# Kernel optimization log

Measured on AMD Instinct MI355X. Metric: run time of the kernel, lower is better.

Reference implementation:

```python
import jax, jax.numpy as jnp
import numpy as np

D = 1024
H = 16
HD = D // H
EPS = 1e-5


def setup_inputs() -> dict:
    key = jax.random.key(0)
    ks = jax.random.split(key, 8)
    s_in = 1.0 / np.sqrt(D)
    s_ff = 1.0 / np.sqrt(4 * D)
    return {
        "x": jax.random.normal(ks[0], (2, 2048, D), dtype=jnp.float32),
        "w_qkv": jax.random.uniform(ks[1], (D, 3 * D), minval=-s_in, maxval=s_in, dtype=jnp.float32),
        "b_qkv": jnp.zeros((3 * D,), jnp.float32),
        "w_out": jax.random.uniform(ks[2], (D, D), minval=-s_in, maxval=s_in, dtype=jnp.float32),
        "b_out": jnp.zeros((D,), jnp.float32),
        "w_ff1": jax.random.uniform(ks[3], (D, 4 * D), minval=-s_in, maxval=s_in, dtype=jnp.float32),
        "b_ff1": jnp.zeros((4 * D,), jnp.float32),
        "w_ff2": jax.random.uniform(ks[4], (4 * D, D), minval=-s_ff, maxval=s_ff, dtype=jnp.float32),
        "b_ff2": jnp.zeros((D,), jnp.float32),
        "gamma1": jnp.ones((D,), jnp.float32),
        "beta1": jnp.zeros((D,), jnp.float32),
        "gamma2": jnp.ones((D,), jnp.float32),
        "beta2": jnp.zeros((D,), jnp.float32),
    }


def _layer_norm(x, gamma, beta):
    mean = jnp.mean(x, axis=-1, keepdims=True)
    var = jnp.var(x, axis=-1, keepdims=True, ddof=1)  # torch.var is unbiased
    return (x - mean) / jnp.sqrt(var + EPS) * gamma + beta


def reference(x, w_qkv, b_qkv, w_out, b_out, w_ff1, b_ff1, w_ff2, b_ff2,
              gamma1, beta1, gamma2, beta2):
    B, C, _ = x.shape
    qkv = x @ w_qkv + b_qkv                     # [B,C,3D]
    q, k, v = jnp.split(qkv, 3, axis=-1)
    # [B,C,D] -> [B,H,C,hd]
    q = q.reshape(B, C, H, HD).transpose(0, 2, 1, 3)
    k = k.reshape(B, C, H, HD).transpose(0, 2, 1, 3)
    v = v.reshape(B, C, H, HD).transpose(0, 2, 1, 3)
    attn = jnp.einsum('bhid,bhjd->bhij', q, k) / np.sqrt(HD).astype(np.float32)
    attn = jax.nn.softmax(attn, axis=-1)
    h_attn = jnp.einsum('bhij,bhjd->bhid', attn, v)
    h_attn = h_attn.transpose(0, 2, 1, 3).reshape(B, C, D)
    h_attn = h_attn @ w_out + b_out
    h_attn = _layer_norm(h_attn + x, gamma1, beta1)
    h_ff = jax.nn.gelu(h_attn @ w_ff1 + b_ff1, approximate=False) @ w_ff2 + b_ff2
    return _layer_norm(h_ff + h_attn, gamma2, beta2)
```

## Files before the change

kernel.cpp:

```cpp
#include <hip/hip_runtime.h>
#include <hip/hip_bf16.h>
#include <math.h>

#define DDIM 1024
#define HHD  64
#define NH   16
#define BB   2
#define CTX  2048
#define MROWS (BB*CTX)
#define D3   (3*DDIM)
#define DF   (4*DDIM)

using bf16x8 = __attribute__((ext_vector_type(8))) short;
using f32x4  = __attribute__((ext_vector_type(4))) float;

__device__ __forceinline__ unsigned short f2bf(float f) {
  union { float f; unsigned u; } c; c.f = f;
  unsigned u = c.u;
  return (unsigned short)((u + 0x7FFFu + ((u >> 16) & 1u)) >> 16);
}

__device__ __forceinline__ unsigned pk2(float a, float b) {
  __hip_bfloat162 h = __float22bfloat162_rn(float2{a, b});
  return *reinterpret_cast<unsigned*>(&h);
}

__device__ __forceinline__ void gload16(const void* g, void* l) {
  __builtin_amdgcn_global_load_lds(
      (const __attribute__((address_space(1))) unsigned int*)g,
      (__attribute__((address_space(3))) unsigned int*)l, 16, 0, 0);
}

template<int N>
__device__ __forceinline__ void vmwait() {
  if constexpr (N == 0)      asm volatile("s_waitcnt vmcnt(0)" ::: "memory");
  else if constexpr (N == 3) asm volatile("s_waitcnt vmcnt(3)" ::: "memory");
  else if constexpr (N == 4) asm volatile("s_waitcnt vmcnt(4)" ::: "memory");
  else static_assert(N != N, "add vmcnt literal");
}

__global__ void k_cvt_bf16(const float* __restrict__ in, unsigned short* __restrict__ out, int n4) {
  int i = blockIdx.x * blockDim.x + threadIdx.x;
  if (i >= n4) return;
  float4 v = reinterpret_cast<const float4*>(in)[i];
  uint2 o;
  o.x = pk2(v.x, v.y); o.y = pk2(v.z, v.w);
  reinterpret_cast<uint2*>(out)[i] = o;
}

__global__ void k_transpose_w(const float* __restrict__ in, unsigned short* __restrict__ out,
                              int R, int Cn) {
  __shared__ float tile[32][33];
  int c0 = blockIdx.x * 32, r0 = blockIdx.y * 32;
  int t = threadIdx.x, tr = t >> 5, tc = t & 31;
#pragma unroll
  for (int i = 0; i < 4; ++i)
    tile[tr + i*8][tc] = in[(size_t)(r0 + tr + i*8) * Cn + (c0 + tc)];
  __syncthreads();
#pragma unroll
  for (int i = 0; i < 4; ++i)
    out[(size_t)(c0 + tr + i*8) * R + (r0 + tc)] = f2bf(tile[tc][tr + i*8]);
}

__global__ void k_transpose_v(const unsigned short* __restrict__ in, unsigned short* __restrict__ out) {
  __shared__ unsigned short tile[32][33];
  int head = blockIdx.z;
  int d0 = blockIdx.x * 32, c0 = blockIdx.y * 32;
  int t = threadIdx.x, tr = t >> 5, tc = t & 31;
  const unsigned short* ip = in + (size_t)head * CTX * HHD;
  unsigned short* op = out + (size_t)head * CTX * HHD;
#pragma unroll
  for (int i = 0; i < 4; ++i)
    tile[tr + i*8][tc] = ip[(c0 + tr + i*8) * HHD + (d0 + tc)];
  __syncthreads();
#pragma unroll
  for (int i = 0; i < 4; ++i)
    op[(d0 + tr + i*8) * CTX + (c0 + tc)] = tile[tc][tr + i*8];
}

template<int EPI, int BM, int BN, int WSM, int WSN, int OCC>
__launch_bounds__(WSM*WSN*64, OCC)
__global__ void k_gemm(const unsigned short* __restrict__ A,
                       const unsigned short* __restrict__ Bt,
                       const float* __restrict__ bias,
                       const float* __restrict__ res,
                       float* __restrict__ outf,
                       unsigned short* __restrict__ outb,
                       unsigned short* __restrict__ outQ,
                       unsigned short* __restrict__ outK,
                       unsigned short* __restrict__ outV,
                       int Ndim, int Kdim) {
  constexpr int THREADS = WSM * WSN * 64;
  constexpr int WM = BM / (WSM * 16);
  constexpr int WN = BN / (WSN * 16);
  constexpr int LA = (BM * 4) / THREADS;
  constexpr int LB = (BN * 4) / THREADS;
  constexpr int L  = LA + LB;
  constexpr int NBUF = 3;

  __shared__ __align__(16) unsigned short As[NBUF][BM * 32];
  __shared__ __align__(16) unsigned short Bs[NBUF][BN * 32];

  const int nwg = gridDim.x * gridDim.y;
  const int lin = blockIdx.y * gridDim.x + blockIdx.x;
  const int swz = (lin & 7) * (nwg >> 3) + (lin >> 3);
  const int m0 = (swz / gridDim.x) * BM, n0 = (swz % gridDim.x) * BN;

  const int t = threadIdx.x;
  const int w = t >> 6, lane = t & 63, lr = lane & 15, lg = lane >> 4;
  const int wr = (w / WSN) * (WM * 16);
  const int wc = (w % WSN) * (WN * 16);

  f32x4 acc[WM][WN];
#pragma unroll
  for (int i = 0; i < WM; ++i)
#pragma unroll
    for (int j = 0; j < WN; ++j) acc[i][j] = f32x4{0.f, 0.f, 0.f, 0.f};

  const int srow = t >> 2;
  const int sgr  = (t & 3) ^ ((t >> 3) & 3);
  const unsigned short* Asrc[LA];
  const unsigned short* Bsrc[LB];
#pragma unroll
  for (int i = 0; i < LA; ++i)
    Asrc[i] = A + (size_t)(m0 + i * (THREADS / 4) + srow) * Kdim + sgr * 8;
#pragma unroll
  for (int i = 0; i < LB; ++i)
    Bsrc[i] = Bt + (size_t)(n0 + i * (THREADS / 4) + srow) * Kdim + sgr * 8;

  int offA[WM], offB[WN];
#pragma unroll
  for (int mi = 0; mi < WM; ++mi) {
    int r = wr + mi * 16 + lr;
    offA[mi] = r * 32 + ((lg ^ ((r >> 1) & 3)) * 8);
  }
#pragma unroll
  for (int ni = 0; ni < WN; ++ni) {
    int r = wc + ni * 16 + lr;
    offB[ni] = r * 32 + ((lg ^ ((r >> 1) & 3)) * 8);
  }

#define STAGE(buf, ko)                                                   \
  do {                                                                   \
    _Pragma("unroll")                                                    \
    for (int i = 0; i < LA; ++i)                                         \
      gload16(Asrc[i] + (ko), &As[buf][(i * THREADS + t) * 8]);          \
    _Pragma("unroll")                                                    \
    for (int i = 0; i < LB; ++i)                                         \
      gload16(Bsrc[i] + (ko), &Bs[buf][(i * THREADS + t) * 8]);          \
  } while (0)

  STAGE(0, 0);
  STAGE(1, 32);

  const int nk = Kdim >> 5;
  int rd = 0, tgt = 2;
  for (int kk = 0; kk < nk; ++kk) {
    if (kk + 1 < nk) vmwait<L>(); else vmwait<0>();
    __builtin_amdgcn_s_barrier();
    asm volatile("" ::: "memory");
    if (kk + 2 < nk) STAGE(tgt, (kk + 2) * 32);

    bf16x8 af[WM], bfr[WN];
#pragma unroll
    for (int mi = 0; mi < WM; ++mi) af[mi]  = *(const bf16x8*)&As[rd][offA[mi]];
#pragma unroll
    for (int ni = 0; ni < WN; ++ni) bfr[ni] = *(const bf16x8*)&Bs[rd][offB[ni]];
    if constexpr (WM >= 8) __builtin_amdgcn_s_setprio(1);
#pragma unroll
    for (int mi = 0; mi < WM; ++mi)
#pragma unroll
      for (int ni = 0; ni < WN; ++ni)
        acc[mi][ni] = __builtin_amdgcn_mfma_f32_16x16x32_bf16(af[mi], bfr[ni], acc[mi][ni], 0, 0, 0);
    if constexpr (WM >= 8) __builtin_amdgcn_s_setprio(0);
    rd  = (rd == 2)  ? 0 : rd + 1;
    tgt = (tgt == 2) ? 0 : tgt + 1;
  }
#undef STAGE

#pragma unroll
  for (int mi = 0; mi < WM; ++mi) {
#pragma unroll
    for (int r = 0; r < 4; ++r) {
      int row = m0 + wr + mi * 16 + lg * 4 + r;
#pragma unroll
      for (int ni = 0; ni < WN; ++ni) {
        int col = n0 + wc + ni * 16 + lr;
        float v = acc[mi][ni][r] + bias[col];
        if constexpr (EPI == 0) {
          int b = row >> 11, c = row & 2047;
          int sec = col >> 10, nn = col & 1023;
          int h = nn >> 6, d = nn & 63;
          size_t o = ((size_t)(b * NH + h) * CTX + c) * HHD + d;
          if (sec == 0) outQ[o] = f2bf(v * 0.18033688f);
          else if (sec == 1) outK[o] = f2bf(v);
          else outV[o] = f2bf(v);
        } else if constexpr (EPI == 1) {
          size_t o = (size_t)row * Ndim + col;
          outf[o] = v + res[o];
        } else {
          float g = 0.5f * v * (1.0f + erff(v * 0.70710678118654752f));
          outb[(size_t)row * Ndim + col] = f2bf(g);
        }
      }
    }
  }
}

__launch_bounds__(256, 4)
__global__ void k_attn(const unsigned short* __restrict__ Qb,
                       const unsigned short* __restrict__ Kb,
                       const unsigned short* __restrict__ Vt,
                       unsigned short* __restrict__ A2) {
  __shared__ __align__(16) unsigned short Ks[2][64 * 64];
  __shared__ __align__(16) unsigned short Vs[2][64 * 64];
  __shared__ __align__(16) unsigned short pls[4][16 * 64];
  const int lin = blockIdx.x;
  const int blk = (lin & 7) * 128 + (lin >> 3);
  const int bh = blk >> 5;
  const int qt = blk & 31;
  const int b = bh >> 4, h = bh & 15;
  const int t = threadIdx.x, w = t >> 6, lane = t & 63, lr = lane & 15, lg = lane >> 4;
  const int qbase = qt * 64 + w * 16;
  const unsigned short* Qh = Qb + (size_t)bh * CTX * HHD;
  const unsigned short* Kh = Kb + (size_t)bh * CTX * HHD;
  const unsigned short* Vh = Vt + (size_t)bh * CTX * HHD;
  unsigned short* pw = pls[w];

  const int srow = t >> 3, sgr = (t & 7) ^ ((t >> 3) & 7);
  const unsigned short* Kg0 = Kh + srow * HHD + sgr * 8;
  const unsigned short* Kg1 = Kg0 + 32 * HHD;
  const unsigned short* Vg0 = Vh + (size_t)srow * CTX + sgr * 8;
  const unsigned short* Vg1 = Vg0 + (size_t)32 * CTX;

#define STAGEKV(buf, j0)                              \
  do {                                                \
    gload16(Kg0 + (j0) * HHD, &Ks[buf][t * 8]);       \
    gload16(Kg1 + (j0) * HHD, &Ks[buf][(256 + t) * 8]); \
    gload16(Vg0 + (j0), &Vs[buf][t * 8]);             \
    gload16(Vg1 + (j0), &Vs[buf][(256 + t) * 8]);     \
  } while (0)

  STAGEKV(0, 0);

  bf16x8 aq[2];
#pragma unroll
  for (int kc = 0; kc < 2; ++kc)
    aq[kc] = *(const bf16x8*)(Qh + (qbase + lr) * HHD + kc * 32 + lg * 8);

  __syncthreads();

  float mrun = -1e30f, lsum = 0.f;
  f32x4 oacc[4];
#pragma unroll
  for (int nt = 0; nt < 4; ++nt) oacc[nt] = f32x4{0.f, 0.f, 0.f, 0.f};

  int cur = 0;
  for (int j0 = 0; j0 < CTX; j0 += 64) {
    if (j0 + 64 < CTX) STAGEKV(cur ^ 1, j0 + 64);

    f32x4 s[4];
#pragma unroll
    for (int nt = 0; nt < 4; ++nt) {
      s[nt] = f32x4{0.f, 0.f, 0.f, 0.f};
#pragma unroll
      for (int kc = 0; kc < 2; ++kc) {
        bf16x8 kf = *(const bf16x8*)&Ks[cur][(nt*16 + lr) * 64 + (((kc*4 + lg) ^ (lr & 7)) * 8)];
        s[nt] = __builtin_amdgcn_mfma_f32_16x16x32_bf16(kf, aq[kc], s[nt], 0, 0, 0);
      }
    }

    f32x4 m4;
#pragma unroll
    for (int r = 0; r < 4; ++r)
      m4[r] = fmaxf(fmaxf(s[0][r], s[1][r]), fmaxf(s[2][r], s[3][r]));
    float pm = fmaxf(fmaxf(m4[0], m4[1]), fmaxf(m4[2], m4[3]));
    if (__any(pm - mrun > 8.0f)) {
      float m = pm;
      m = fmaxf(m, __shfl_xor(m, 16));
      m = fmaxf(m, __shfl_xor(m, 32));
      float mn = fmaxf(mrun, m);
      float alpha = __builtin_amdgcn_exp2f(mrun - mn);
      mrun = mn;
      lsum *= alpha;
#pragma unroll
      for (int nt = 0; nt < 4; ++nt) oacc[nt] *= alpha;
    }
#pragma unroll
    for (int nt = 0; nt < 4; ++nt)
#pragma unroll
      for (int r = 0; r < 4; ++r)
        s[nt][r] = __builtin_amdgcn_exp2f(s[nt][r] - mrun);
    f32x4 s4 = (s[0] + s[1]) + (s[2] + s[3]);
    lsum += (s4[0] + s4[1]) + (s4[2] + s4[3]);

#pragma unroll
    for (int nt = 0; nt < 4; ++nt) {
      uint2 pk;
      pk.x = pk2(s[nt][0], s[nt][1]);
      pk.y = pk2(s[nt][2], s[nt][3]);
      int G = nt * 2 + (lg >> 1);
      *(uint2*)&pw[lr * 64 + ((G ^ (lr & 7)) * 8) + (lg & 1) * 4] = pk;
    }
    bf16x8 pf[2];
#pragma unroll
    for (int kc = 0; kc < 2; ++kc)
      pf[kc] = *(const bf16x8*)&pw[lr * 64 + (((kc*4 + lg) ^ (lr & 7)) * 8)];
#pragma unroll
    for (int nt = 0; nt < 4; ++nt) {
#pragma unroll
      for (int kc = 0; kc < 2; ++kc) {
        bf16x8 vf = *(const bf16x8*)&Vs[cur][(nt*16 + lr) * 64 + (((kc*4 + lg) ^ (lr & 7)) * 8)];
        oacc[nt] = __builtin_amdgcn_mfma_f32_16x16x32_bf16(vf, pf[kc], oacc[nt], 0, 0, 0);
      }
    }
    __syncthreads();
    cur ^= 1;
  }
#undef STAGEKV

  lsum += __shfl_xor(lsum, 16);
  lsum += __shfl_xor(lsum, 32);
  float rinv = 1.0f / lsum;
  size_t rowoff = ((size_t)(b * CTX + qbase + lr)) * DDIM + h * HHD;
#pragma unroll
  for (int nt = 0; nt < 4; ++nt) {
    uint2 ov;
    ov.x = pk2(oacc[nt][0] * rinv, oacc[nt][1] * rinv);
    ov.y = pk2(oacc[nt][2] * rinv, oacc[nt][3] * rinv);
    *(uint2*)&A2[rowoff + nt * 16 + lg * 4] = ov;
  }
}

template<bool WB>
__global__ void k_ln(const float* __restrict__ in, const float* __restrict__ gamma,
                     const float* __restrict__ beta, float* __restrict__ outf,
                     unsigned short* __restrict__ outb) {
  const int row = blockIdx.x, t = threadIdx.x;
  float4 v = reinterpret_cast<const float4*>(in + (size_t)row * DDIM)[t];
  float s  = (v.x + v.y) + (v.z + v.w);
  float sq = (v.x*v.x + v.y*v.y) + (v.z*v.z + v.w*v.w);
#pragma unroll
  for (int off = 1; off < 64; off <<= 1) { s += __shfl_xor(s, off); sq += __shfl_xor(sq, off); }
  __shared__ float red[2][4];
  int w = t >> 6;
  if ((t & 63) == 0) { red[0][w] = s; red[1][w] = sq; }
  __syncthreads();
  s  = red[0][0] + red[0][1] + red[0][2] + red[0][3];
  sq = red[1][0] + red[1][1] + red[1][2] + red[1][3];
  float mean = s * (1.0f / DDIM);
  float var  = (sq - s * mean) * (1.0f / (DDIM - 1));
  float rstd = rsqrtf(var + 1e-5f);
  float4 gm = reinterpret_cast<const float4*>(gamma)[t];
  float4 bt = reinterpret_cast<const float4*>(beta)[t];
  float4 o;
  o.x = (v.x - mean) * rstd * gm.x + bt.x;
  o.y = (v.y - mean) * rstd * gm.y + bt.y;
  o.z = (v.z - mean) * rstd * gm.z + bt.z;
  o.w = (v.w - mean) * rstd * gm.w + bt.w;
  reinterpret_cast<float4*>(outf + (size_t)row * DDIM)[t] = o;
  if constexpr (WB) {
    uint2 p; p.x = pk2(o.x, o.y); p.y = pk2(o.z, o.w);
    reinterpret_cast<uint2*>(outb + (size_t)row * DDIM)[t] = p;
  }
}

extern "C" void kernel_launch(void* const* d_in, const int* in_sizes, int n_in,
                              void* d_out, int out_size, void* d_ws, size_t ws_size,
                              hipStream_t stream) {
  const float* x      = (const float*)d_in[0];
  const float* w_qkv  = (const float*)d_in[1];
  const float* b_qkv  = (const float*)d_in[2];
  const float* w_out  = (const float*)d_in[3];
  const float* b_out  = (const float*)d_in[4];
  const float* w_ff1  = (const float*)d_in[5];
  const float* b_ff1  = (const float*)d_in[6];
  const float* w_ff2  = (const float*)d_in[7];
  const float* b_ff2  = (const float*)d_in[8];
  const float* gamma1 = (const float*)d_in[9];
  const float* beta1  = (const float*)d_in[10];
  const float* gamma2 = (const float*)d_in[11];
  const float* beta2  = (const float*)d_in[12];
  float* out = (float*)d_out;

  char* ws = (char*)d_ws;
  const size_t MB = 1024ull * 1024ull;
  unsigned short* Xb    = (unsigned short*)(ws + 0);
  unsigned short* WqkvT = (unsigned short*)(ws + 8*MB);
  unsigned short* WoutT = (unsigned short*)(ws + 14*MB);
  unsigned short* Wff1T = (unsigned short*)(ws + 16*MB);
  unsigned short* Wff2T = (unsigned short*)(ws + 24*MB);
  unsigned short* Qb    = (unsigned short*)(ws + 32*MB);
  unsigned short* Kb    = (unsigned short*)(ws + 40*MB);
  unsigned short* Vt    = (unsigned short*)(ws + 48*MB);
  unsigned short* A2    = (unsigned short*)(ws + 56*MB);
  unsigned short* Vb    = (unsigned short*)(ws + 56*MB);
  unsigned short* G     = (unsigned short*)(ws + 32*MB);
  float* y1             = (float*)(ws + 64*MB);
  float* z              = (float*)(ws + 64*MB);
  float* h1f            = (float*)(ws + 80*MB);
  unsigned short* h1b   = (unsigned short*)(ws + 96*MB);

  k_cvt_bf16<<<dim3(MROWS*DDIM/4/256), dim3(256), 0, stream>>>(x, Xb, MROWS*DDIM/4);
  k_transpose_w<<<dim3(D3/32,  DDIM/32), dim3(256), 0, stream>>>(w_qkv, WqkvT, DDIM, D3);
  k_transpose_w<<<dim3(DDIM/32, DDIM/32), dim3(256), 0, stream>>>(w_out, WoutT, DDIM, DDIM);
  k_transpose_w<<<dim3(DF/32,  DDIM/32), dim3(256), 0, stream>>>(w_ff1, Wff1T, DDIM, DF);
  k_transpose_w<<<dim3(DDIM/32, DF/32),  dim3(256), 0, stream>>>(w_ff2, Wff2T, DF, DDIM);

  k_gemm<0, 128, 128, 2, 2, 3><<<dim3(D3/128, MROWS/128), dim3(256), 0, stream>>>(
      Xb, WqkvT, b_qkv, nullptr, nullptr, nullptr, Qb, Kb, Vb, D3, DDIM);
  k_transpose_v<<<dim3(HHD/32, CTX/32, BB*NH), dim3(256), 0, stream>>>(Vb, Vt);

  k_attn<<<dim3(BB*NH*(CTX/64)), dim3(256), 0, stream>>>(Qb, Kb, Vt, A2);

  k_gemm<1, 64, 128, 1, 4, 4><<<dim3(DDIM/128, MROWS/64), dim3(256), 0, stream>>>(
      A2, WoutT, b_out, x, y1, nullptr, nullptr, nullptr, nullptr, DDIM, DDIM);
  k_ln<true><<<dim3(MROWS), dim3(256), 0, stream>>>(y1, gamma1, beta1, h1f, h1b);

  k_gemm<2, 256, 256, 2, 4, 2><<<dim3(DF/256, MROWS/256), dim3(512), 0, stream>>>(
      h1b, Wff1T, b_ff1, nullptr, nullptr, G, nullptr, nullptr, nullptr, DF, DDIM);
  k_gemm<1, 64, 128, 1, 4, 4><<<dim3(DDIM/128, MROWS/64), dim3(256), 0, stream>>>(
      G, Wff2T, b_ff2, h1f, z, nullptr, nullptr, nullptr, nullptr, DDIM, DF);
  k_ln<false><<<dim3(MROWS), dim3(256), 0, stream>>>(z, gamma2, beta2, out, nullptr);
}
```

Baseline: 280.8 us.

## Split-K the out-projection and FF2 GEMMs and fuse the reduction into LayerNorm

The two N=1024 GEMMs (out-projection and FF2) now use 128x128 tiles with a two-way K split across blockIdx.z. Each split writes its fp32 partial to a separate workspace buffer. The LayerNorm kernels sum the two partials, add bias and residual, then normalize. This raises the block count for these GEMMs to fill the GPU better with larger tiles, at the cost of an extra fp32 partial buffer written and read, and workspace aliasing that must not clobber live data.

New measurement: 272.6 us. 1.03x faster.

```diff
diff --git a/kernel.cpp b/kernel.cpp
--- a/kernel.cpp
+++ b/kernel.cpp
@@ -78,7 +78,7 @@
     op[(d0 + tr + i*8) * CTX + (c0 + tc)] = tile[tc][tr + i*8];
 }
 
-template<int EPI, int BM, int BN, int WSM, int WSN, int OCC>
+template<int EPI, int BM, int BN, int WSM, int WSN, int OCC, int SPLITK = 1>
 __launch_bounds__(WSM*WSN*64, OCC)
 __global__ void k_gemm(const unsigned short* __restrict__ A,
                        const unsigned short* __restrict__ Bt,
@@ -106,6 +106,9 @@
   const int swz = (lin & 7) * (nwg >> 3) + (lin >> 3);
   const int m0 = (swz / gridDim.x) * BM, n0 = (swz % gridDim.x) * BN;
 
+  const int Kc = Kdim / SPLITK;
+  const size_t koff = (size_t)blockIdx.z * Kc;
+
   const int t = threadIdx.x;
   const int w = t >> 6, lane = t & 63, lr = lane & 15, lg = lane >> 4;
   const int wr = (w / WSN) * (WM * 16);
@@ -123,10 +126,10 @@
   const unsigned short* Bsrc[LB];
 #pragma unroll
   for (int i = 0; i < LA; ++i)
-    Asrc[i] = A + (size_t)(m0 + i * (THREADS / 4) + srow) * Kdim + sgr * 8;
+    Asrc[i] = A + (size_t)(m0 + i * (THREADS / 4) + srow) * Kdim + koff + sgr * 8;
 #pragma unroll
   for (int i = 0; i < LB; ++i)
-    Bsrc[i] = Bt + (size_t)(n0 + i * (THREADS / 4) + srow) * Kdim + sgr * 8;
+    Bsrc[i] = Bt + (size_t)(n0 + i * (THREADS / 4) + srow) * Kdim + koff + sgr * 8;
 
   int offA[WM], offB[WN];
 #pragma unroll
@@ -153,7 +156,7 @@
   STAGE(0, 0);
   STAGE(1, 32);
 
-  const int nk = Kdim >> 5;
+  const int nk = Kc >> 5;
   int rd = 0, tgt = 2;
   for (int kk = 0; kk < nk; ++kk) {
     if (kk + 1 < nk) vmwait<L>(); else vmwait<0>();
@@ -178,6 +181,10 @@
   }
 #undef STAGE
 
+  float* cpw = nullptr;
+  if constexpr (EPI == 3)
+    cpw = (blockIdx.z == 0) ? outf : (float*)outb;
+
 #pragma unroll
   for (int mi = 0; mi < WM; ++mi) {
 #pragma unroll
@@ -186,7 +193,8 @@
 #pragma unroll
       for (int ni = 0; ni < WN; ++ni) {
         int col = n0 + wc + ni * 16 + lr;
-        float v = acc[mi][ni][r] + bias[col];
+        float v = acc[mi][ni][r];
+        if constexpr (EPI != 3) v += bias[col];
         if constexpr (EPI == 0) {
           int b = row >> 11, c = row & 2047;
           int sec = col >> 10, nn = col & 1023;
@@ -198,9 +206,11 @@
         } else if constexpr (EPI == 1) {
           size_t o = (size_t)row * Ndim + col;
           outf[o] = v + res[o];
-        } else {
+        } else if constexpr (EPI == 2) {
           float g = 0.5f * v * (1.0f + erff(v * 0.70710678118654752f));
           outb[(size_t)row * Ndim + col] = f2bf(g);
+        } else {
+          cpw[(size_t)row * Ndim + col] = v;
         }
       }
     }
@@ -333,11 +343,21 @@
 }
 
 template<bool WB>
-__global__ void k_ln(const float* __restrict__ in, const float* __restrict__ gamma,
-                     const float* __restrict__ beta, float* __restrict__ outf,
-                     unsigned short* __restrict__ outb) {
+__global__ void k_lnred(const float* __restrict__ cp0, const float* __restrict__ cp1,
+                        const float* __restrict__ bias, const float* __restrict__ res,
+                        const float* __restrict__ gamma, const float* __restrict__ beta,
+                        float* __restrict__ outf, unsigned short* __restrict__ outb) {
   const int row = blockIdx.x, t = threadIdx.x;
-  float4 v = reinterpret_cast<const float4*>(in + (size_t)row * DDIM)[t];
+  const size_t o4 = (size_t)row * (DDIM / 4) + t;
+  float4 a  = reinterpret_cast<const float4*>(cp0)[o4];
+  float4 bq = reinterpret_cast<const float4*>(cp1)[o4];
+  float4 rr = reinterpret_cast<const float4*>(res)[o4];
+  float4 bi = reinterpret_cast<const float4*>(bias)[t];
+  float4 v;
+  v.x = a.x + bq.x + bi.x + rr.x;
+  v.y = a.y + bq.y + bi.y + rr.y;
+  v.z = a.z + bq.z + bi.z + rr.z;
+  v.w = a.w + bq.w + bi.w + rr.w;
   float s  = (v.x + v.y) + (v.z + v.w);
   float sq = (v.x*v.x + v.y*v.y) + (v.z*v.z + v.w*v.w);
 #pragma unroll
@@ -396,10 +416,12 @@
   unsigned short* A2    = (unsigned short*)(ws + 56*MB);
   unsigned short* Vb    = (unsigned short*)(ws + 56*MB);
   unsigned short* G     = (unsigned short*)(ws + 32*MB);
-  float* y1             = (float*)(ws + 64*MB);
-  float* z              = (float*)(ws + 64*MB);
-  float* h1f            = (float*)(ws + 80*MB);
-  unsigned short* h1b   = (unsigned short*)(ws + 96*MB);
+  float* h1f            = (float*)(ws + 64*MB);
+  unsigned short* h1b   = (unsigned short*)(ws + 80*MB);
+  float* Cp1a           = (float*)(ws + 88*MB);
+  float* Cp1b           = (float*)(ws + 32*MB);
+  float* Cp2a           = (float*)(ws + 0);
+  float* Cp2b           = (float*)(ws + 88*MB);
 
   k_cvt_bf16<<<dim3(MROWS*DDIM/4/256), dim3(256), 0, stream>>>(x, Xb, MROWS*DDIM/4);
   k_transpose_w<<<dim3(D3/32,  DDIM/32), dim3(256), 0, stream>>>(w_qkv, WqkvT, DDIM, D3);
@@ -413,13 +435,18 @@
 
   k_attn<<<dim3(BB*NH*(CTX/64)), dim3(256), 0, stream>>>(Qb, Kb, Vt, A2);
 
-  k_gemm<1, 64, 128, 1, 4, 4><<<dim3(DDIM/128, MROWS/64), dim3(256), 0, stream>>>(
-      A2, WoutT, b_out, x, y1, nullptr, nullptr, nullptr, nullptr, DDIM, DDIM);
-  k_ln<true><<<dim3(MROWS), dim3(256), 0, stream>>>(y1, gamma1, beta1, h1f, h1b);
+  k_gemm<3, 128, 128, 2, 2, 3, 2><<<dim3(DDIM/128, MROWS/128, 2), dim3(256), 0, stream>>>(
+      A2, WoutT, nullptr, nullptr, Cp1a, (unsigned short*)Cp1b, nullptr, nullptr, nullptr,
+      DDIM, DDIM);
+  k_lnred<true><<<dim3(MROWS), dim3(256), 0, stream>>>(
+      Cp1a, Cp1b, b_out, x, gamma1, beta1, h1f, h1b);
 
   k_gemm<2, 256, 256, 2, 4, 2><<<dim3(DF/256, MROWS/256), dim3(512), 0, stream>>>(
       h1b, Wff1T, b_ff1, nullptr, nullptr, G, nullptr, nullptr, nullptr, DF, DDIM);
-  k_gemm<1, 64, 128, 1, 4, 4><<<dim3(DDIM/128, MROWS/64), dim3(256), 0, stream>>>(
-      G, Wff2T, b_ff2, h1f, z, nullptr, nullptr, nullptr, nullptr, DDIM, DF);
-  k_ln<false><<<dim3(MROWS), dim3(256), 0, stream>>>(z, gamma2, beta2, out, nullptr);
-}
+
+  k_gemm<3, 128, 128, 2, 2, 3, 2><<<dim3(DDIM/128, MROWS/128, 2), dim3(256), 0, stream>>>(
+      G, Wff2T, nullptr, nullptr, Cp2a, (unsigned short*)Cp2b, nullptr, nullptr, nullptr,
+      DDIM, DF);
+  k_lnred<false><<<dim3(MROWS), dim3(256), 0, stream>>>(
+      Cp2a, Cp2b, b_ff2, h1f, gamma2, beta2, out, nullptr);
+}
```
